# Optimization experiments

Hardware: AMD Instinct MI355X
Metric: run time of the kernel (lower is better)

Reference implementation:

```python
import jax, jax.numpy as jnp
import numpy as np

N = 203769
E = 234355
IN, HID, OUT = 165, 128, 64
EPS = 1e-5


def setup_inputs() -> dict:
    key = jax.random.key(0)
    ks = jax.random.split(key, 12)
    x = jax.random.normal(ks[0], (N, IN), dtype=jnp.float32)
    edge_index = jax.random.randint(ks[1], (2, E), 0, N, dtype=jnp.int64)
    s = lambda fan: 1.0 / np.sqrt(fan)
    W1 = jax.random.uniform(ks[2], (IN, HID), jnp.float32, -s(IN), s(IN))
    b1 = jnp.zeros((HID,), jnp.float32)
    g1 = jnp.ones((HID,), jnp.float32)
    be1 = jnp.zeros((HID,), jnp.float32)
    W2 = jax.random.uniform(ks[3], (HID, OUT), jnp.float32, -s(HID), s(HID))
    b2 = jnp.zeros((OUT,), jnp.float32)
    g2 = jnp.ones((OUT,), jnp.float32)
    be2 = jnp.zeros((OUT,), jnp.float32)
    Wp1 = jax.random.uniform(ks[4], (OUT, OUT), jnp.float32, -s(OUT), s(OUT))
    bp1 = jax.random.uniform(ks[5], (OUT,), jnp.float32, -s(OUT), s(OUT))
    Wp2 = jax.random.uniform(ks[6], (OUT, OUT), jnp.float32, -s(OUT), s(OUT))
    bp2 = jax.random.uniform(ks[7], (OUT,), jnp.float32, -s(OUT), s(OUT))
    return {"x": x, "edge_index": edge_index, "W1": W1, "b1": b1, "g1": g1, "be1": be1,
            "W2": W2, "b2": b2, "g2": g2, "be2": be2,
            "Wp1": Wp1, "bp1": bp1, "Wp2": Wp2, "bp2": bp2}


def gcn_conv(x, W, b, src, dst, n):
    # PyG GCNConv: h = xW; add self-loops; sym-normalized aggregation; + bias
    h = x @ W  # [N, F]
    loop = jnp.arange(n, dtype=src.dtype)
    s = jnp.concatenate([src, loop])
    d = jnp.concatenate([dst, loop])
    w = jnp.ones(s.shape[0], x.dtype)  # edge_weight=None -> ones
    deg = jax.ops.segment_sum(w, d, num_segments=n)
    dinv = jnp.where(deg > 0, jax.lax.rsqrt(deg), 0.0)
    norm = dinv[s] * w * dinv[d]  # [E+N]
    msg = h[s] * norm[:, None]    # gather + scale
    return jax.ops.segment_sum(msg, d, num_segments=n) + b


def batch_norm(x, g, be):
    m = jnp.mean(x, axis=0)
    v = jnp.mean(jnp.square(x - m), axis=0)  # biased var (torch BN)
    return (x - m) * jax.lax.rsqrt(v + EPS) * g + be


def reference(x, edge_index, W1, b1, g1, be1, W2, b2, g2, be2, Wp1, bp1, Wp2, bp2):
    src, dst = edge_index[0], edge_index[1]
    n = x.shape[0]
    h = gcn_conv(x, W1, b1, src, dst, n)
    h = jax.nn.relu(batch_norm(h, g1, be1))  # dropout omitted (eval / deterministic)
    h = gcn_conv(h, W2, b2, src, dst, n)
    h = batch_norm(h, g2, be2)  # last layer: no relu/dropout
    z = jax.nn.relu(h @ Wp1 + bp1) @ Wp2 + bp2
    return (h, z)
```

## Files before the change

### kernel.cpp

```cpp
#include <hip/hip_runtime.h>
#include <hip/hip_bf16.h>

#define N_NODES 203769
#define N_EDGES 234355
#define F_IN    165
#define F_HID   128
#define F_OUT   64
#define BN_EPS  1e-5f
#define NB_SCAN 796
#define KP      192
#define NBLK    1024
#define GB128C  1593
#define RGP     (GB128C * 8)

typedef short bf16x8 __attribute__((ext_vector_type(8)));
typedef unsigned short u16x8 __attribute__((ext_vector_type(8)));
typedef float f32x4 __attribute__((ext_vector_type(4)));

__device__ __forceinline__ unsigned short f2bf(float f) {
    unsigned int u = __builtin_bit_cast(unsigned int, f);
    u += 0x7fffu + ((u >> 16) & 1u);
    return (unsigned short)(u >> 16);
}
__device__ __forceinline__ float bf2f(unsigned short h) {
    unsigned int u = ((unsigned int)h) << 16;
    return __builtin_bit_cast(float, u);
}

__global__ void k_count(const int* __restrict__ dst, int* __restrict__ cnt) {
    int e = blockIdx.x * 256 + threadIdx.x;
    if (e < N_EDGES) atomicAdd(&cnt[dst[e]], 1);
}

__global__ __launch_bounds__(256) void k_scanA(const int* __restrict__ cnt,
                                               int* __restrict__ partials) {
    __shared__ int sm[256];
    int t = threadIdx.x;
    int i = blockIdx.x * 256 + t;
    int v = (i < N_NODES) ? cnt[i] : 0;
    sm[t] = v;
    __syncthreads();
    for (int off = 128; off > 0; off >>= 1) {
        if (t < off) sm[t] += sm[t + off];
        __syncthreads();
    }
    if (t == 0) partials[blockIdx.x] = sm[0];
}

__global__ __launch_bounds__(1024) void k_scanB(int* __restrict__ partials,
                                                int* __restrict__ row_ptr) {
    __shared__ int sm[1024];
    int t = threadIdx.x;
    int v = (t < NB_SCAN) ? partials[t] : 0;
    sm[t] = v;
    __syncthreads();
    for (int off = 1; off < 1024; off <<= 1) {
        int add = (t >= off) ? sm[t - off] : 0;
        __syncthreads();
        sm[t] += add;
        __syncthreads();
    }
    if (t < NB_SCAN) partials[t] = sm[t] - v;
    if (t == NB_SCAN - 1) row_ptr[N_NODES] = sm[t];
}

__global__ __launch_bounds__(256) void k_scanC(const int* __restrict__ cnt,
                                               const int* __restrict__ partials,
                                               int* __restrict__ row_ptr,
                                               int* __restrict__ cursor,
                                               float* __restrict__ dinv) {
    __shared__ int sm[256];
    int t = threadIdx.x;
    int i = blockIdx.x * 256 + t;
    int v = (i < N_NODES) ? cnt[i] : 0;
    sm[t] = v;
    __syncthreads();
    for (int off = 1; off < 256; off <<= 1) {
        int add = (t >= off) ? sm[t - off] : 0;
        __syncthreads();
        sm[t] += add;
        __syncthreads();
    }
    if (i < N_NODES) {
        int p = partials[blockIdx.x] + sm[t] - v;
        row_ptr[i] = p;
        cursor[i] = p;
        dinv[i] = rsqrtf(1.0f + (float)v);
    }
}

__global__ void k_scatter(const int* __restrict__ src, const int* __restrict__ dst,
                          int* __restrict__ cursor, int* __restrict__ csr_src) {
    int e = blockIdx.x * 256 + threadIdx.x;
    if (e < N_EDGES) {
        int pos = atomicAdd(&cursor[dst[e]], 1);
        csr_src[pos] = src[e];
    }
}

__global__ void k_cvt_w(const float* __restrict__ W1, unsigned short* __restrict__ wb) {
    int i = blockIdx.x * 256 + threadIdx.x;
    if (i < F_HID * KP) {
        int n = i / KP, k = i - n * KP;
        float v = (k < F_IN) ? W1[k * F_HID + n] : 0.0f;
        int ng = n >> 4, l16 = n & 15, kb = k >> 5, quad = (k >> 3) & 3, j = k & 7;
        wb[((((size_t)ng * 6 + kb) * 4 + quad) * 16 + l16) * 8 + j] = f2bf(v);
    }
}

__global__ void k_cvt_w2(const float* __restrict__ W2,
                         unsigned short* __restrict__ w2h,
                         unsigned short* __restrict__ w2l) {
    int i = blockIdx.x * 256 + threadIdx.x;
    if (i < F_HID * F_OUT) {
        int k = i / F_OUT, n = i - k * F_OUT;
        float v = W2[i];
        unsigned short h = f2bf(v);
        float lo = v - bf2f(h);
        int ng = n >> 4, l16 = n & 15, kb = k >> 5, quad = (k >> 3) & 3, j = k & 7;
        size_t idx = ((((size_t)ng * 4 + kb) * 4 + quad) * 16 + l16) * 8 + j;
        w2h[idx] = h;
        w2l[idx] = f2bf(lo);
    }
}

__global__ __launch_bounds__(256) void k_cvt_x(const float* __restrict__ x,
                                               unsigned short* __restrict__ xa) {
    __shared__ unsigned short xt[16 * 200];
    const int rg = blockIdx.x;
    const int t = threadIdx.x;
    const int row0 = rg * 16;

    if (row0 + 16 <= N_NODES) {
        const float* slab = x + (size_t)row0 * F_IN;
        for (int u = t; u < 660; u += 256) {
            float4 v = *(const float4*)&slab[u * 4];
            float vv[4] = {v.x, v.y, v.z, v.w};
            int f0 = u * 4;
#pragma unroll
            for (int j = 0; j < 4; j++) {
                int f = f0 + j;
                int r = f / 165;
                int k = f - r * 165;
                xt[r * 200 + k] = f2bf(vv[j]);
            }
        }
    } else {
        for (int u = t; u < 660; u += 256) {
            int f0 = u * 4;
#pragma unroll
            for (int j = 0; j < 4; j++) {
                int f = f0 + j;
                int r = f / 165;
                int k = f - r * 165;
                int row = row0 + r;
                float val = (row < N_NODES) ? x[(size_t)row * F_IN + k] : 0.0f;
                xt[r * 200 + k] = f2bf(val);
            }
        }
    }
    __syncthreads();

    for (int v = t; v < 384; v += 256) {
        int l16 = v & 15;
        int quad = (v >> 4) & 3;
        int kb = v >> 6;
        int k0 = kb * 32 + quad * 8;
        u16x8 uv;
#pragma unroll
        for (int j = 0; j < 8; j++) {
            int k = k0 + j;
            uv[j] = (k < F_IN) ? xt[l16 * 200 + k] : (unsigned short)0;
        }
        *(u16x8*)&xa[((size_t)rg * 384 + v) * 8] = uv;
    }
}

__global__ __launch_bounds__(256) void k_mfma1(const unsigned short* __restrict__ xa,
                                               const unsigned short* __restrict__ wb,
                                               const float* __restrict__ dinv,
                                               float* __restrict__ h1s) {
    const int t = threadIdx.x;
    const int wv = t >> 6;
    const int lane = t & 63;
    const int l16 = lane & 15;
    const int quad = lane >> 4;
    const int rg0 = blockIdx.x * 8 + wv * 2;
    const int lq = quad * 16 + l16;

    f32x4 acc[2][8];
#pragma unroll
    for (int mt = 0; mt < 2; mt++)
#pragma unroll
        for (int nt = 0; nt < 8; nt++)
            acc[mt][nt] = (f32x4){0.0f, 0.0f, 0.0f, 0.0f};

#pragma unroll
    for (int kb = 0; kb < 6; kb++) {
        bf16x8 a[2], b[8];
#pragma unroll
        for (int mt = 0; mt < 2; mt++)
            a[mt] = *(const bf16x8*)&xa[(((size_t)(rg0 + mt) * 6 + kb) * 64 + lq) * 8];
#pragma unroll
        for (int nt = 0; nt < 8; nt++)
            b[nt] = *(const bf16x8*)&wb[(((size_t)nt * 6 + kb) * 64 + lq) * 8];
#pragma unroll
        for (int mt = 0; mt < 2; mt++)
#pragma unroll
            for (int nt = 0; nt < 8; nt++)
                acc[mt][nt] = __builtin_amdgcn_mfma_f32_16x16x32_bf16(
                    a[mt], b[nt], acc[mt][nt], 0, 0, 0);
    }

#pragma unroll
    for (int mt = 0; mt < 2; mt++) {
#pragma unroll
        for (int rgi = 0; rgi < 4; rgi++) {
            int grow = (rg0 + mt) * 16 + quad * 4 + rgi;
            if (grow < N_NODES) {
                float dv = dinv[grow];
                float* orow = h1s + (size_t)grow * F_HID + l16;
#pragma unroll
                for (int nt = 0; nt < 8; nt++)
                    orow[nt * 16] = acc[mt][nt][rgi] * dv;
            }
        }
    }
}

__global__ __launch_bounds__(256) void k_mfma2(const float* __restrict__ out1,
                                               const float* __restrict__ sc1,
                                               const float* __restrict__ sh1,
                                               const unsigned short* __restrict__ w2h,
                                               const unsigned short* __restrict__ w2l,
                                               const float* __restrict__ dinv,
                                               float* __restrict__ h2s) {
    const int t = threadIdx.x;
    const int wv = t >> 6;
    const int lane = t & 63;
    const int l16 = lane & 15;
    const int quad = lane >> 4;
    const int rg0 = blockIdx.x * 8 + wv * 2;
    const int lq = quad * 16 + l16;

    f32x4 acc[2][4];
#pragma unroll
    for (int mt = 0; mt < 2; mt++)
#pragma unroll
        for (int nt = 0; nt < 4; nt++)
            acc[mt][nt] = (f32x4){0.0f, 0.0f, 0.0f, 0.0f};

#pragma unroll
    for (int kb = 0; kb < 4; kb++) {
        const int k0 = kb * 32 + quad * 8;
        float4 sA = *(const float4*)&sc1[k0];
        float4 sB = *(const float4*)&sc1[k0 + 4];
        float4 hA = *(const float4*)&sh1[k0];
        float4 hB = *(const float4*)&sh1[k0 + 4];
        float sv[8] = {sA.x, sA.y, sA.z, sA.w, sB.x, sB.y, sB.z, sB.w};
        float hv[8] = {hA.x, hA.y, hA.z, hA.w, hB.x, hB.y, hB.z, hB.w};

        bf16x8 bh[4], bl[4];
#pragma unroll
        for (int nt = 0; nt < 4; nt++) {
            size_t u = ((((size_t)nt * 4 + kb) * 64) + lq) * 8;
            bh[nt] = *(const bf16x8*)&w2h[u];
            bl[nt] = *(const bf16x8*)&w2l[u];
        }

        bf16x8 ah[2], al[2];
#pragma unroll
        for (int mt = 0; mt < 2; mt++) {
            int row = (rg0 + mt) * 16 + l16;
            float v[8];
            if (row < N_NODES) {
                const float* rp = out1 + (size_t)row * F_HID + k0;
                float4 v0 = *(const float4*)rp;
                float4 v1 = *(const float4*)(rp + 4);
                v[0] = v0.x; v[1] = v0.y; v[2] = v0.z; v[3] = v0.w;
                v[4] = v1.x; v[5] = v1.y; v[6] = v1.z; v[7] = v1.w;
            } else {
#pragma unroll
                for (int j = 0; j < 8; j++) v[j] = 0.0f;
            }
            u16x8 uh, ul;
#pragma unroll
            for (int j = 0; j < 8; j++) {
                float f = fmaxf(fmaf(v[j], sv[j], hv[j]), 0.0f);
                unsigned short hb = f2bf(f);
                uh[j] = hb;
                ul[j] = f2bf(f - bf2f(hb));
            }
            ah[mt] = __builtin_bit_cast(bf16x8, uh);
            al[mt] = __builtin_bit_cast(bf16x8, ul);
        }

#pragma unroll
        for (int mt = 0; mt < 2; mt++)
#pragma unroll
            for (int nt = 0; nt < 4; nt++) {
                acc[mt][nt] = __builtin_amdgcn_mfma_f32_16x16x32_bf16(
                    ah[mt], bh[nt], acc[mt][nt], 0, 0, 0);
                acc[mt][nt] = __builtin_amdgcn_mfma_f32_16x16x32_bf16(
                    al[mt], bh[nt], acc[mt][nt], 0, 0, 0);
                acc[mt][nt] = __builtin_amdgcn_mfma_f32_16x16x32_bf16(
                    ah[mt], bl[nt], acc[mt][nt], 0, 0, 0);
            }
    }

#pragma unroll
    for (int mt = 0; mt < 2; mt++) {
#pragma unroll
        for (int rgi = 0; rgi < 4; rgi++) {
            int grow = (rg0 + mt) * 16 + quad * 4 + rgi;
            if (grow < N_NODES) {
                float dv = dinv[grow];
                float* orow = h2s + (size_t)grow * F_OUT + l16;
#pragma unroll
                for (int nt = 0; nt < 4; nt++)
                    orow[nt * 16] = acc[mt][nt][rgi] * dv;
            }
        }
    }
}

template <int C, int TPN, int NPB>
__global__ __launch_bounds__(256) void k_aggr(const float* __restrict__ hs,
                                              const int* __restrict__ row_ptr,
                                              const int* __restrict__ csr_src,
                                              const float* __restrict__ dinv,
                                              float* __restrict__ out,
                                              float* __restrict__ psum,
                                              float* __restrict__ psq) {
    const int t = threadIdx.x;
    const int q = t & (TPN - 1);
    const int slot = t / TPN;
    float s0 = 0, s1 = 0, s2 = 0, s3 = 0;
    float q0 = 0, q1 = 0, q2 = 0, q3 = 0;

    for (int node = blockIdx.x * NPB + slot; node < N_NODES;
         node += gridDim.x * NPB) {
        int beg = row_ptr[node];
        int end = row_ptr[node + 1];
        float4 acc = *(const float4*)&hs[(size_t)node * C + q * 4];
        for (int e = beg; e < end; e++) {
            int s = csr_src[e];
            float4 v = *(const float4*)&hs[(size_t)s * C + q * 4];
            acc.x += v.x; acc.y += v.y; acc.z += v.z; acc.w += v.w;
        }
        float dv = dinv[node];
        acc.x *= dv; acc.y *= dv; acc.z *= dv; acc.w *= dv;
        *(float4*)&out[(size_t)node * C + q * 4] = acc;
        s0 += acc.x; s1 += acc.y; s2 += acc.z; s3 += acc.w;
        q0 = fmaf(acc.x, acc.x, q0); q1 = fmaf(acc.y, acc.y, q1);
        q2 = fmaf(acc.z, acc.z, q2); q3 = fmaf(acc.w, acc.w, q3);
    }

    __shared__ float sm[256 * 4];
    __shared__ float sq[256 * 4];
    sm[t * 4 + 0] = s0; sm[t * 4 + 1] = s1; sm[t * 4 + 2] = s2; sm[t * 4 + 3] = s3;
    sq[t * 4 + 0] = q0; sq[t * 4 + 1] = q1; sq[t * 4 + 2] = q2; sq[t * 4 + 3] = q3;
    __syncthreads();
    if (t < TPN) {
#pragma unroll
        for (int sl = 1; sl < NPB; sl++) {
            int u = (sl * TPN + t) * 4;
            s0 += sm[u + 0]; s1 += sm[u + 1]; s2 += sm[u + 2]; s3 += sm[u + 3];
            q0 += sq[u + 0]; q1 += sq[u + 1]; q2 += sq[u + 2]; q3 += sq[u + 3];
        }
        float4 o1 = {s0, s1, s2, s3};
        float4 o2 = {q0, q1, q2, q3};
        *(float4*)&psum[(size_t)blockIdx.x * C + t * 4] = o1;
        *(float4*)&psq [(size_t)blockIdx.x * C + t * 4] = o2;
    }
}

template <int C>
__global__ __launch_bounds__(1024) void k_bn_fin(const float* __restrict__ psum,
                                                 const float* __restrict__ psq,
                                                 const float* __restrict__ g,
                                                 const float* __restrict__ be,
                                                 float* __restrict__ sc,
                                                 float* __restrict__ sh) {
    const int t = threadIdx.x;
    const int c = t & (C - 1);
    const int gg = t / C;
    const int G = 1024 / C;
    const int BPG = NBLK / G;
    float s = 0.0f, sq_ = 0.0f;
    for (int i = 0; i < BPG; i++) {
        int b = gg * BPG + i;
        s   += psum[(size_t)b * C + c];
        sq_ += psq [(size_t)b * C + c];
    }
    __shared__ float sm[1024];
    __shared__ float s2[1024];
    sm[t] = s;
    s2[t] = sq_;
    __syncthreads();
    for (int off = G / 2; off > 0; off >>= 1) {
        if (gg < off) {
            sm[t] += sm[t + off * C];
            s2[t] += s2[t + off * C];
        }
        __syncthreads();
    }
    if (gg == 0) {
        const float invn = 1.0f / (float)N_NODES;
        float mean = sm[c] * invn;
        float var = s2[c] * invn - mean * mean;
        float rstd = rsqrtf(var + BN_EPS);
        float scale = g[c] * rstd;
        sc[c] = scale;
        sh[c] = fmaf(-mean, scale, be[c]);
    }
}

__global__ __launch_bounds__(256) void k_final(const float* __restrict__ out2,
                                               const float* __restrict__ sc2,
                                               const float* __restrict__ sh2,
                                               const float* __restrict__ Wp1,
                                               const float* __restrict__ bp1,
                                               const float* __restrict__ Wp2,
                                               const float* __restrict__ bp2,
                                               float* __restrict__ out) {
    __shared__ float hs[64 * 68];
    __shared__ float as_[64 * 68];
    const int row0 = blockIdx.x * 64;
    const int t = threadIdx.x;

    {
        const float4* src = (const float4*)out2;
        float4* dsth = (float4*)out;
#pragma unroll
        for (int i = 0; i < 4; i++) {
            int f4 = t + i * 256;
            int r = f4 >> 4;
            int c4 = f4 & 15;
            int grow = row0 + r;
            float4 v = {0, 0, 0, 0};
            if (grow < N_NODES) v = src[(size_t)grow * 16 + c4];
            int c = c4 * 4;
            v.x = fmaf(v.x, sc2[c + 0], sh2[c + 0]);
            v.y = fmaf(v.y, sc2[c + 1], sh2[c + 1]);
            v.z = fmaf(v.z, sc2[c + 2], sh2[c + 2]);
            v.w = fmaf(v.w, sc2[c + 3], sh2[c + 3]);
            if (grow < N_NODES) dsth[(size_t)grow * 16 + c4] = v;
            *(float4*)&hs[r * 68 + c] = v;
        }
    }
    __syncthreads();

    const int c0 = (t & 15) * 4;
    const int r0 = (t >> 4) * 4;

    {
        float acc[4][4];
#pragma unroll
        for (int r = 0; r < 4; r++)
#pragma unroll
            for (int c = 0; c < 4; c++) acc[r][c] = 0.0f;
#pragma unroll 2
        for (int k4 = 0; k4 < 64; k4 += 4) {
            float4 xv[4];
#pragma unroll
            for (int r = 0; r < 4; r++)
                xv[r] = *(const float4*)&hs[(r0 + r) * 68 + k4];
            float4 w[4];
#pragma unroll
            for (int j = 0; j < 4; j++)
                w[j] = *(const float4*)&Wp1[(k4 + j) * 64 + c0];
#pragma unroll
            for (int r = 0; r < 4; r++) {
                const float xr[4] = {xv[r].x, xv[r].y, xv[r].z, xv[r].w};
#pragma unroll
                for (int j = 0; j < 4; j++) {
                    acc[r][0] = fmaf(xr[j], w[j].x, acc[r][0]);
                    acc[r][1] = fmaf(xr[j], w[j].y, acc[r][1]);
                    acc[r][2] = fmaf(xr[j], w[j].z, acc[r][2]);
                    acc[r][3] = fmaf(xr[j], w[j].w, acc[r][3]);
                }
            }
        }
        float4 b = *(const float4*)&bp1[c0];
#pragma unroll
        for (int r = 0; r < 4; r++) {
            float4 o = {fmaxf(acc[r][0] + b.x, 0.0f), fmaxf(acc[r][1] + b.y, 0.0f),
                        fmaxf(acc[r][2] + b.z, 0.0f), fmaxf(acc[r][3] + b.w, 0.0f)};
            *(float4*)&as_[(r0 + r) * 68 + c0] = o;
        }
    }
    __syncthreads();

    {
        float acc[4][4];
#pragma unroll
        for (int r = 0; r < 4; r++)
#pragma unroll
            for (int c = 0; c < 4; c++) acc[r][c] = 0.0f;
#pragma unroll 2
        for (int k4 = 0; k4 < 64; k4 += 4) {
            float4 xv[4];
#pragma unroll
            for (int r = 0; r < 4; r++)
                xv[r] = *(const float4*)&as_[(r0 + r) * 68 + k4];
            float4 w[4];
#pragma unroll
            for (int j = 0; j < 4; j++)
                w[j] = *(const float4*)&Wp2[(k4 + j) * 64 + c0];
#pragma unroll
            for (int r = 0; r < 4; r++) {
                const float xr[4] = {xv[r].x, xv[r].y, xv[r].z, xv[r].w};
#pragma unroll
                for (int j = 0; j < 4; j++) {
                    acc[r][0] = fmaf(xr[j], w[j].x, acc[r][0]);
                    acc[r][1] = fmaf(xr[j], w[j].y, acc[r][1]);
                    acc[r][2] = fmaf(xr[j], w[j].z, acc[r][2]);
                    acc[r][3] = fmaf(xr[j], w[j].w, acc[r][3]);
                }
            }
        }
        float4 b = *(const float4*)&bp2[c0];
        float* zout = out + (size_t)N_NODES * 64;
#pragma unroll
        for (int r = 0; r < 4; r++) {
            int row = row0 + r0 + r;
            if (row < N_NODES) {
                float4 o = {acc[r][0] + b.x, acc[r][1] + b.y,
                            acc[r][2] + b.z, acc[r][3] + b.w};
                *(float4*)&zout[(size_t)row * 64 + c0] = o;
            }
        }
    }
}

extern "C" void kernel_launch(void* const* d_in, const int* in_sizes, int n_in,
                              void* d_out, int out_size, void* d_ws, size_t ws_size,
                              hipStream_t stream) {
    const float* x   = (const float*)d_in[0];
    const int*   ei  = (const int*)d_in[1];
    const float* W1  = (const float*)d_in[2];
    const float* g1  = (const float*)d_in[4];
    const float* be1 = (const float*)d_in[5];
    const float* W2  = (const float*)d_in[6];
    const float* g2  = (const float*)d_in[8];
    const float* be2 = (const float*)d_in[9];
    const float* Wp1 = (const float*)d_in[10];
    const float* bp1 = (const float*)d_in[11];
    const float* Wp2 = (const float*)d_in[12];
    const float* bp2 = (const float*)d_in[13];

    const int* src = ei;
    const int* dst = ei + N_EDGES;

    float* ws = (float*)d_ws;
    float* A    = ws;
    float* B    = A + (size_t)N_NODES * 128;
    float* dinv = B + (size_t)N_NODES * 128;
    float* st   = dinv + N_NODES;
    float* sc1  = st + 256;  float* sh1  = st + 384;
    float* sc2  = st + 640;  float* sh2  = st + 704;
    int* cnt      = (int*)(st + 768);
    int* row_ptr  = cnt + N_NODES;
    int* cursor   = row_ptr + N_NODES + 1;
    int* csr_src  = cursor + N_NODES;
    int* partials = csr_src + N_EDGES;
    unsigned short* wb = (unsigned short*)(partials + NB_SCAN);
    unsigned short* w2h = wb + (size_t)F_HID * KP;
    unsigned short* w2l = w2h + (size_t)F_HID * F_OUT;

    size_t off = (size_t)((char*)(w2l + F_HID * F_OUT) - (char*)d_ws);
    off = (off + 15) & ~(size_t)15;
    float* ps1  = (float*)((char*)d_ws + off);
    float* ps1q = ps1 + (size_t)NBLK * 128;
    float* ps2  = ps1q + (size_t)NBLK * 128;
    float* ps2q = ps2 + (size_t)NBLK * 64;
    unsigned short* xa = (unsigned short*)(ps2q + (size_t)NBLK * 64);

    hipMemsetAsync(st, 0, (768 + N_NODES) * sizeof(float), stream);

    const int EB = (N_EDGES + 255) / 256;
    const int GB64 = (N_NODES + 63) / 64;

    k_count<<<EB, 256, 0, stream>>>(dst, cnt);
    k_cvt_w<<<(F_HID * KP + 255) / 256, 256, 0, stream>>>(W1, wb);
    k_cvt_w2<<<(F_HID * F_OUT + 255) / 256, 256, 0, stream>>>(W2, w2h, w2l);
    k_cvt_x<<<RGP, 256, 0, stream>>>(x, xa);
    k_scanA<<<NB_SCAN, 256, 0, stream>>>(cnt, partials);
    k_scanB<<<1, 1024, 0, stream>>>(partials, row_ptr);
    k_scanC<<<NB_SCAN, 256, 0, stream>>>(cnt, partials, row_ptr, cursor, dinv);
    k_scatter<<<EB, 256, 0, stream>>>(src, dst, cursor, csr_src);

    k_mfma1<<<GB128C, 256, 0, stream>>>(xa, wb, dinv, A);
    k_aggr<128, 32, 8><<<NBLK, 256, 0, stream>>>(A, row_ptr, csr_src, dinv, B, ps1, ps1q);
    k_bn_fin<128><<<1, 1024, 0, stream>>>(ps1, ps1q, g1, be1, sc1, sh1);

    k_mfma2<<<GB128C, 256, 0, stream>>>(B, sc1, sh1, w2h, w2l, dinv, A);
    k_aggr<64, 16, 16><<<NBLK, 256, 0, stream>>>(A, row_ptr, csr_src, dinv, B, ps2, ps2q);
    k_bn_fin<64><<<1, 1024, 0, stream>>>(ps2, ps2q, g2, be2, sc2, sh2);

    k_final<<<GB64, 256, 0, stream>>>(B, sc2, sh2, Wp1, bp1, Wp2, bp2, (float*)d_out);
}
```

Baseline: 546.7 us.

## Fuse fp32-to-bf16 conversion of x into first MFMA GEMM and raise aggregation blocks

Removes the separate k_cvt_x pass that wrote a packed bf16 copy of x. The first GEMM kernel now reads fp32 rows of x directly with unaligned 16-byte loads and converts them to bf16 in registers. This drops one full write and reread of the converted input, at the cost of strided per-row fp32 loads inside the GEMM, where the rows of 165 floats are not 16-byte aligned. The number of aggregation blocks also rises from 1024 to 4096, which gives more parallelism but enlarges the batch-norm partial-sum arrays that the finalize kernels must reduce.

After: 682.0 us. 24.7% more time.

```diff
diff --git a/kernel.cpp b/kernel.cpp
--- a/kernel.cpp
+++ b/kernel.cpp
@@ -9,13 +9,13 @@
 #define BN_EPS  1e-5f
 #define NB_SCAN 796
 #define KP      192
-#define NBLK    1024
+#define NBLK    4096
 #define GB128C  1593
-#define RGP     (GB128C * 8)
 
 typedef short bf16x8 __attribute__((ext_vector_type(8)));
 typedef unsigned short u16x8 __attribute__((ext_vector_type(8)));
 typedef float f32x4 __attribute__((ext_vector_type(4)));
+typedef float f32x4u __attribute__((ext_vector_type(4), aligned(4)));
 
 __device__ __forceinline__ unsigned short f2bf(float f) {
     unsigned int u = __builtin_bit_cast(unsigned int, f);
@@ -124,59 +124,7 @@
     }
 }
 
-__global__ __launch_bounds__(256) void k_cvt_x(const float* __restrict__ x,
-                                               unsigned short* __restrict__ xa) {
-    __shared__ unsigned short xt[16 * 200];
-    const int rg = blockIdx.x;
-    const int t = threadIdx.x;
-    const int row0 = rg * 16;
-
-    if (row0 + 16 <= N_NODES) {
-        const float* slab = x + (size_t)row0 * F_IN;
-        for (int u = t; u < 660; u += 256) {
-            float4 v = *(const float4*)&slab[u * 4];
-            float vv[4] = {v.x, v.y, v.z, v.w};
-            int f0 = u * 4;
-#pragma unroll
-            for (int j = 0; j < 4; j++) {
-                int f = f0 + j;
-                int r = f / 165;
-                int k = f - r * 165;
-                xt[r * 200 + k] = f2bf(vv[j]);
-            }
-        }
-    } else {
-        for (int u = t; u < 660; u += 256) {
-            int f0 = u * 4;
-#pragma unroll
-            for (int j = 0; j < 4; j++) {
-                int f = f0 + j;
-                int r = f / 165;
-                int k = f - r * 165;
-                int row = row0 + r;
-                float val = (row < N_NODES) ? x[(size_t)row * F_IN + k] : 0.0f;
-                xt[r * 200 + k] = f2bf(val);
-            }
-        }
-    }
-    __syncthreads();
-
-    for (int v = t; v < 384; v += 256) {
-        int l16 = v & 15;
-        int quad = (v >> 4) & 3;
-        int kb = v >> 6;
-        int k0 = kb * 32 + quad * 8;
-        u16x8 uv;
-#pragma unroll
-        for (int j = 0; j < 8; j++) {
-            int k = k0 + j;
-            uv[j] = (k < F_IN) ? xt[l16 * 200 + k] : (unsigned short)0;
-        }
-        *(u16x8*)&xa[((size_t)rg * 384 + v) * 8] = uv;
-    }
-}
-
-__global__ __launch_bounds__(256) void k_mfma1(const unsigned short* __restrict__ xa,
+__global__ __launch_bounds__(256) void k_mfma1(const float* __restrict__ x,
                                                const unsigned short* __restrict__ wb,
                                                const float* __restrict__ dinv,
                                                float* __restrict__ h1s) {
@@ -197,10 +145,34 @@
 
 #pragma unroll
     for (int kb = 0; kb < 6; kb++) {
+        const int k0 = kb * 32 + quad * 8;
         bf16x8 a[2], b[8];
 #pragma unroll
-        for (int mt = 0; mt < 2; mt++)
-            a[mt] = *(const bf16x8*)&xa[(((size_t)(rg0 + mt) * 6 + kb) * 64 + lq) * 8];
+        for (int mt = 0; mt < 2; mt++) {
+            int row = (rg0 + mt) * 16 + l16;
+            u16x8 u;
+            if (row < N_NODES) {
+                const float* rp = x + (size_t)row * F_IN + k0;
+                if (kb < 5) {
+                    f32x4u v0 = *(const f32x4u*)rp;
+                    f32x4u v1 = *(const f32x4u*)(rp + 4);
+                    u[0] = f2bf(v0[0]); u[1] = f2bf(v0[1]);
+                    u[2] = f2bf(v0[2]); u[3] = f2bf(v0[3]);
+                    u[4] = f2bf(v1[0]); u[5] = f2bf(v1[1]);
+                    u[6] = f2bf(v1[2]); u[7] = f2bf(v1[3]);
+                } else {
+#pragma unroll
+                    for (int j = 0; j < 8; j++) {
+                        int k = k0 + j;
+                        u[j] = (k < F_IN) ? f2bf(rp[j]) : (unsigned short)0;
+                    }
+                }
+            } else {
+#pragma unroll
+                for (int j = 0; j < 8; j++) u[j] = 0;
+            }
+            a[mt] = __builtin_bit_cast(bf16x8, u);
+        }
 #pragma unroll
         for (int nt = 0; nt < 8; nt++)
             b[nt] = *(const bf16x8*)&wb[(((size_t)nt * 6 + kb) * 64 + lq) * 8];
@@ -575,7 +547,6 @@
     float* ps1q = ps1 + (size_t)NBLK * 128;
     float* ps2  = ps1q + (size_t)NBLK * 128;
     float* ps2q = ps2 + (size_t)NBLK * 64;
-    unsigned short* xa = (unsigned short*)(ps2q + (size_t)NBLK * 64);
 
     hipMemsetAsync(st, 0, (768 + N_NODES) * sizeof(float), stream);
 
@@ -585,13 +556,12 @@
     k_count<<<EB, 256, 0, stream>>>(dst, cnt);
     k_cvt_w<<<(F_HID * KP + 255) / 256, 256, 0, stream>>>(W1, wb);
     k_cvt_w2<<<(F_HID * F_OUT + 255) / 256, 256, 0, stream>>>(W2, w2h, w2l);
-    k_cvt_x<<<RGP, 256, 0, stream>>>(x, xa);
     k_scanA<<<NB_SCAN, 256, 0, stream>>>(cnt, partials);
     k_scanB<<<1, 1024, 0, stream>>>(partials, row_ptr);
     k_scanC<<<NB_SCAN, 256, 0, stream>>>(cnt, partials, row_ptr, cursor, dinv);
     k_scatter<<<EB, 256, 0, stream>>>(src, dst, cursor, csr_src);
 
-    k_mfma1<<<GB128C, 256, 0, stream>>>(xa, wb, dinv, A);
+    k_mfma1<<<GB128C, 256, 0, stream>>>(x, wb, dinv, A);
     k_aggr<128, 32, 8><<<NBLK, 256, 0, stream>>>(A, row_ptr, csr_src, dinv, B, ps1, ps1q);
     k_bn_fin<128><<<1, 1024, 0, stream>>>(ps1, ps1q, g1, be1, sc1, sh1);
 
```
